# Optimization experiments

Hardware: AMD Instinct MI355X
Metric: run time of the kernel (lower is better)

The kernel has to match this reference:

```python
import jax, jax.numpy as jnp
import numpy as np

N_NODES = 50000  # nodes in the (sub)graph


def setup_inputs() -> dict:
    key = jax.random.key(0)
    ks = jax.random.split(key, 8)
    nodes = jax.random.randint(ks[0], (N_NODES,), 0, 100000)
    src = jax.random.randint(ks[1], (800000,), 0, N_NODES)
    dst = jax.random.randint(ks[2], (800000,), 0, N_NODES)
    emb = jax.random.normal(ks[3], (100000, 256), dtype=jnp.float32)
    W = jax.random.normal(ks[4], (256, 128), dtype=jnp.float32) * 0.05
    b = jax.random.normal(ks[5], (128,), dtype=jnp.float32) * 0.05
    mlp_w = jax.random.normal(ks[6], (128, 40), dtype=jnp.float32) * 0.05
    mlp_b = jax.random.normal(ks[7], (40,), dtype=jnp.float32) * 0.05
    return {"nodes": nodes, "src": src, "dst": dst, "emb": emb,
            "W": W, "b": b, "mlp_w": mlp_w, "mlp_b": mlp_b}


def reference(nodes, src, dst, emb, W, b, mlp_w, mlp_b):
    n = N_NODES
    ones = jnp.ones_like(src, dtype=jnp.float32)
    out_deg = jax.ops.segment_sum(ones, src, num_segments=n)  # src out-degree
    in_deg = jax.ops.segment_sum(ones, dst, num_segments=n)   # dst in-degree
    norm_src = jax.lax.rsqrt(jnp.maximum(out_deg, 1.0))       # D_out^{-1/2}
    norm_dst = jax.lax.rsqrt(jnp.maximum(in_deg, 1.0))        # D_in^{-1/2}

    feat = emb[nodes]                                          # [N, in_dim]
    # dgl GraphConv(norm='both'): in_dim > out_dim -> project first, then aggregate
    h = (feat * norm_src[:, None]) @ W                         # [N, out_dim]
    agg = jax.ops.segment_sum(h[src], dst, num_segments=n)     # SpMM: sum over in-edges
    feat_out = agg * norm_dst[:, None] + b                     # [N, out_dim]

    logits = feat_out @ mlp_w + mlp_b                          # [N, num_classes]
    return (feat_out, logits)
```

## Files before the change

kernel.cpp:

```cpp
#include <hip/hip_runtime.h>

#define IN_DIM 256
#define OUT_DIM 128
#define N_CLS 40

#define SLICE 16384
#define NE_CH 40

typedef __attribute__((ext_vector_type(8))) short short8;
typedef __attribute__((ext_vector_type(4))) float floatx4;

static __device__ __forceinline__ unsigned short f2bf(float f) {
    union { float f; unsigned u; } v; v.f = f;
    unsigned r = v.u + 0x7FFF + ((v.u >> 16) & 1);
    return (unsigned short)(r >> 16);
}

static __device__ __forceinline__ unsigned cvtpk(float lo, float hi) {
    unsigned r;
    asm("v_cvt_pk_bf16_f32 %0, %1, %2" : "=v"(r) : "v"(lo), "v"(hi));
    return r;
}

__global__ __launch_bounds__(256) void hist_wconv_kernel(
    const int* __restrict__ src, const int* __restrict__ dst,
    int* __restrict__ partial_out, int* __restrict__ partial_in,
    const float* __restrict__ W, unsigned short* __restrict__ Wt,
    int ne, int n, int chunk, int nbh)
{
    __shared__ __align__(16) int lh_out[SLICE];
    __shared__ __align__(16) int lh_in[SLICE];

    const int tid = threadIdx.x;

    if (blockIdx.x >= nbh) {
        int t = (blockIdx.x - nbh) * 256 + tid;
        if (t < IN_DIM * OUT_DIM) {
            int k = t >> 7, c = t & 127;
            Wt[c * IN_DIM + k] = f2bf(W[t]);
        }
        return;
    }

    const int s = blockIdx.x / NE_CH;
    const int e = blockIdx.x % NE_CH;
    const int lo = s * SLICE;
    const int hi = min(lo + SLICE, n);

    for (int i = tid; i < SLICE; i += 256) { lh_out[i] = 0; lh_in[i] = 0; }
    __syncthreads();

    const int start = e * chunk;
    const int end = min(start + chunk, ne);
    const int cnt4 = (end - start) >> 2;
    const int4* s4 = (const int4*)(src + start);
    const int4* d4 = (const int4*)(dst + start);
    for (int k = tid; k < cnt4; k += 256) {
        int4 sv = s4[k];
        int4 dv = d4[k];
        unsigned q;
        q = (unsigned)(sv.x - lo); if (q < SLICE) atomicAdd(&lh_out[q], 1);
        q = (unsigned)(sv.y - lo); if (q < SLICE) atomicAdd(&lh_out[q], 1);
        q = (unsigned)(sv.z - lo); if (q < SLICE) atomicAdd(&lh_out[q], 1);
        q = (unsigned)(sv.w - lo); if (q < SLICE) atomicAdd(&lh_out[q], 1);
        q = (unsigned)(dv.x - lo); if (q < SLICE) atomicAdd(&lh_in[q], 1);
        q = (unsigned)(dv.y - lo); if (q < SLICE) atomicAdd(&lh_in[q], 1);
        q = (unsigned)(dv.z - lo); if (q < SLICE) atomicAdd(&lh_in[q], 1);
        q = (unsigned)(dv.w - lo); if (q < SLICE) atomicAdd(&lh_in[q], 1);
    }
    for (int t = start + (cnt4 << 2) + tid; t < end; t += 256) {
        unsigned q;
        q = (unsigned)(src[t] - lo); if (q < SLICE) atomicAdd(&lh_out[q], 1);
        q = (unsigned)(dst[t] - lo); if (q < SLICE) atomicAdd(&lh_in[q], 1);
    }
    __syncthreads();

    const int cnt = hi - lo;
    const int c4 = cnt >> 2;
    int4* po = (int4*)(partial_out + (size_t)e * n + lo);
    int4* pi = (int4*)(partial_in + (size_t)e * n + lo);
    for (int i = tid; i < c4; i += 256) {
        po[i] = ((const int4*)lh_out)[i];
        pi[i] = ((const int4*)lh_in)[i];
    }
    for (int i = (c4 << 2) + tid; i < cnt; i += 256) {
        partial_out[(size_t)e * n + lo + i] = lh_out[i];
        partial_in[(size_t)e * n + lo + i] = lh_in[i];
    }
}

__global__ __launch_bounds__(256) void reduce_scan_kernel(
    int* __restrict__ partial_out, int* __restrict__ partial_in,
    int* __restrict__ cnt_out, int* __restrict__ row_start,
    int* __restrict__ bsum, int* __restrict__ boffs,
    int* __restrict__ done, int n)
{
    __shared__ int wsum[4];
    __shared__ int is_last;
    const int tid = threadIdx.x;
    const int lane = tid & 63, wid = tid >> 6;
    const int base = blockIdx.x * 1024 + tid * 4;

    int4 run = make_int4(0, 0, 0, 0);

    if (base + 4 <= n) {
        int4 sum = make_int4(0, 0, 0, 0);
#pragma unroll
        for (int e = 0; e < NE_CH; e++) {
            int4 v = *(const int4*)(partial_out + (size_t)e * n + base);
            sum.x += v.x; sum.y += v.y; sum.z += v.z; sum.w += v.w;
        }
        *(int4*)(cnt_out + base) = sum;

#pragma unroll
        for (int e = 0; e < NE_CH; e++) {
            int* p = partial_in + (size_t)e * n + base;
            int4 v = *(const int4*)p;
            *(int4*)p = run;
            run.x += v.x; run.y += v.y; run.z += v.z; run.w += v.w;
        }
    } else if (base <= n) {
        int rr[4] = {0, 0, 0, 0};
#pragma unroll
        for (int j = 0; j < 4; j++) {
            int pos = base + j;
            if (pos < n) {
                int sum = 0, r = 0;
                for (int e = 0; e < NE_CH; e++) {
                    sum += partial_out[(size_t)e * n + pos];
                    int v = partial_in[(size_t)e * n + pos];
                    partial_in[(size_t)e * n + pos] = r;
                    r += v;
                }
                cnt_out[pos] = sum;
                rr[j] = r;
            }
        }
        run.x = rr[0]; run.y = rr[1]; run.z = rr[2]; run.w = rr[3];
    }

    const int s = run.x + run.y + run.z + run.w;
    const int e1 = run.x, e2 = run.x + run.y, e3 = run.x + run.y + run.z;

    int incl = s;
#pragma unroll
    for (int off = 1; off < 64; off <<= 1) {
        int q = __shfl_up(incl, (unsigned)off, 64);
        if (lane >= off) incl += q;
    }
    if (lane == 63) wsum[wid] = incl;
    __syncthreads();
    int woff = 0;
    for (int w = 0; w < wid; ++w) woff += wsum[w];
    const int texcl = woff + incl - s;

    if (base + 4 <= n) {
        int4 o = make_int4(texcl, texcl + e1, texcl + e2, texcl + e3);
        *(int4*)(row_start + base) = o;
    } else if (base <= n) {
        const int eo[4] = {0, e1, e2, e3};
#pragma unroll
        for (int j = 0; j < 4; j++) {
            int pos = base + j;
            if (pos <= n) row_start[pos] = texcl + eo[j];
        }
    }
    if (tid == 0) bsum[blockIdx.x] = wsum[0] + wsum[1] + wsum[2] + wsum[3];

    __threadfence();
    if (tid == 0) {
        int prev = atomicAdd(done, 1);
        is_last = (prev == (int)gridDim.x - 1) ? 1 : 0;
    }
    __syncthreads();
    if (is_last && tid < 64) {
        __threadfence();
        const int nb = (int)gridDim.x;
        int carry = 0;
        for (int c = 0; c < nb; c += 64) {
            int i = c + lane;
            int v = (i < nb) ? bsum[i] : 0;
            int inc2 = v;
#pragma unroll
            for (int off = 1; off < 64; off <<= 1) {
                int q = __shfl_up(inc2, (unsigned)off, 64);
                if (lane >= off) inc2 += q;
            }
            if (i < nb) boffs[i] = carry + inc2 - v;
            carry += __shfl(inc2, 63, 64);
        }
        if (lane == 0) boffs[nb] = carry;
    }
}

__global__ __launch_bounds__(256) void scatter_lds_kernel(
    const int* __restrict__ src, const int* __restrict__ dst,
    const int* __restrict__ row_start, const int* __restrict__ boffs,
    const int* __restrict__ prefix_in,
    int* __restrict__ csr_src, int ne, int n, int chunk)
{
    __shared__ __align__(16) int cur[SLICE];

    const int tid = threadIdx.x;
    const int s = blockIdx.x / NE_CH;
    const int e = blockIdx.x % NE_CH;
    const int lo = s * SLICE;
    const int hi = min(lo + SLICE, n);
    const int cnt = hi - lo;

    const int c4 = cnt >> 2;
    for (int i = tid; i < c4; i += 256) {
        int idx4 = lo + i * 4;
        int4 rs = *(const int4*)(row_start + idx4);
        int4 pf = *(const int4*)(prefix_in + (size_t)e * n + idx4);
        const int bo = boffs[idx4 >> 10];
        rs.x += pf.x + bo; rs.y += pf.y + bo;
        rs.z += pf.z + bo; rs.w += pf.w + bo;
        ((int4*)cur)[i] = rs;
    }
    for (int i = (c4 << 2) + tid; i < cnt; i += 256) {
        int pos = lo + i;
        cur[i] = row_start[pos] + boffs[pos >> 10]
               + prefix_in[(size_t)e * n + pos];
    }
    __syncthreads();

    const int start = e * chunk;
    const int end = min(start + chunk, ne);
    const int cnt4e = (end - start) >> 2;
    const int4* s4 = (const int4*)(src + start);
    const int4* d4 = (const int4*)(dst + start);
    for (int k = tid; k < cnt4e; k += 256) {
        int4 sv = s4[k];
        int4 dv = d4[k];
        unsigned q;
        q = (unsigned)(dv.x - lo); if (q < SLICE) csr_src[atomicAdd(&cur[q], 1)] = sv.x;
        q = (unsigned)(dv.y - lo); if (q < SLICE) csr_src[atomicAdd(&cur[q], 1)] = sv.y;
        q = (unsigned)(dv.z - lo); if (q < SLICE) csr_src[atomicAdd(&cur[q], 1)] = sv.z;
        q = (unsigned)(dv.w - lo); if (q < SLICE) csr_src[atomicAdd(&cur[q], 1)] = sv.w;
    }
    for (int t = start + (cnt4e << 2) + tid; t < end; t += 256) {
        unsigned q = (unsigned)(dst[t] - lo);
        if (q < SLICE) csr_src[atomicAdd(&cur[q], 1)] = src[t];
    }
}

__global__ __launch_bounds__(256) void gemm1_mfma_kernel(
    const int* __restrict__ nodes, const float* __restrict__ emb,
    const unsigned short* __restrict__ Wt, const int* __restrict__ cnt_out,
    unsigned short* __restrict__ h, int n)
{
    __shared__ unsigned short A_lds[128 * 40];
    __shared__ unsigned short B_lds[128 * 40];
    __shared__ int   snode[128];
    __shared__ float sscale[128];

    const int tid = threadIdx.x;
    const int m0  = blockIdx.x * 128;

    if (tid < 128) {
        int gr = m0 + tid;
        snode[tid]  = (gr < n) ? nodes[gr] : 0;
        sscale[tid] = (gr < n) ? rsqrtf(fmaxf((float)cnt_out[gr], 1.0f)) : 0.0f;
    }
    __syncthreads();

    const int arow = tid >> 1, aq = tid & 1;
    const float* aptr = emb + (size_t)snode[arow] * IN_DIM + aq * 16;
    const unsigned short* bptr = Wt + arow * IN_DIM + aq * 16;

    float    ar[16];
    unsigned bw[8];

#define LOAD_REGS(KK) do {                                           \
        _Pragma("unroll")                                            \
        for (int q = 0; q < 4; q++) {                                \
            const floatx4 v = *(const floatx4*)(aptr + (KK) * 32 + q * 4); \
            ar[q*4+0]=v[0]; ar[q*4+1]=v[1]; ar[q*4+2]=v[2]; ar[q*4+3]=v[3]; \
        }                                                            \
        const uint4 w0 = *(const uint4*)(bptr + (KK) * 32);          \
        const uint4 w1 = *(const uint4*)(bptr + (KK) * 32 + 8);      \
        bw[0]=w0.x; bw[1]=w0.y; bw[2]=w0.z; bw[3]=w0.w;              \
        bw[4]=w1.x; bw[5]=w1.y; bw[6]=w1.z; bw[7]=w1.w;              \
    } while (0)

#define WRITE_LDS() do {                                             \
        uint4 uv0, uv1;                                              \
        uv0.x = cvtpk(ar[0],  ar[1]);  uv0.y = cvtpk(ar[2],  ar[3]); \
        uv0.z = cvtpk(ar[4],  ar[5]);  uv0.w = cvtpk(ar[6],  ar[7]); \
        uv1.x = cvtpk(ar[8],  ar[9]);  uv1.y = cvtpk(ar[10], ar[11]);\
        uv1.z = cvtpk(ar[12], ar[13]); uv1.w = cvtpk(ar[14], ar[15]);\
        *(uint4*)&A_lds[arow * 40 + aq * 16]     = uv0;              \
        *(uint4*)&A_lds[arow * 40 + aq * 16 + 8] = uv1;              \
        uint4 b0, b1;                                                \
        b0.x=bw[0]; b0.y=bw[1]; b0.z=bw[2]; b0.w=bw[3];              \
        b1.x=bw[4]; b1.y=bw[5]; b1.z=bw[6]; b1.w=bw[7];              \
        *(uint4*)&B_lds[arow * 40 + aq * 16]     = b0;               \
        *(uint4*)&B_lds[arow * 40 + aq * 16 + 8] = b1;               \
    } while (0)

    const int wave = tid >> 6, lane = tid & 63;
    const int wr = (wave & 1) * 64;
    const int wc = (wave >> 1) * 64;
    const int fr = lane & 15;
    const int koff = (lane >> 4) * 8;

    floatx4 acc[4][4];
#pragma unroll
    for (int i = 0; i < 4; i++)
#pragma unroll
        for (int j = 0; j < 4; j++) acc[i][j] = (floatx4){0.f, 0.f, 0.f, 0.f};

    LOAD_REGS(0);
    WRITE_LDS();

    for (int kk = 0; kk < 8; ++kk) {
        if (kk < 7) LOAD_REGS(kk + 1);
        __syncthreads();
        short8 af[4], bf[4];
#pragma unroll
        for (int t = 0; t < 4; t++) {
            af[t] = *(const short8*)&A_lds[(wr + t * 16 + fr) * 40 + koff];
            bf[t] = *(const short8*)&B_lds[(wc + t * 16 + fr) * 40 + koff];
        }
#pragma unroll
        for (int rt = 0; rt < 4; rt++)
#pragma unroll
            for (int ct = 0; ct < 4; ct++)
                acc[rt][ct] = __builtin_amdgcn_mfma_f32_16x16x32_bf16(
                    bf[ct], af[rt], acc[rt][ct], 0, 0, 0);
        __syncthreads();
        if (kk < 7) WRITE_LDS();
    }

#pragma unroll
    for (int rt = 0; rt < 4; rt++) {
        int lrow = wr + rt * 16 + fr;
        int grow = m0 + lrow;
        float sc = sscale[lrow];
        if (grow < n) {
#pragma unroll
            for (int ct = 0; ct < 4; ct++) {
                int col = wc + ct * 16 + (lane >> 4) * 4;
                uint2 o;
                o.x = cvtpk(acc[rt][ct][0] * sc, acc[rt][ct][1] * sc);
                o.y = cvtpk(acc[rt][ct][2] * sc, acc[rt][ct][3] * sc);
                *(uint2*)&h[(size_t)grow * OUT_DIM + col] = o;
            }
        }
    }
#undef LOAD_REGS
#undef WRITE_LDS
}

__global__ __launch_bounds__(256) void spmm_csr_kernel(
    const int* __restrict__ row_start, const int* __restrict__ boffs,
    const int* __restrict__ csr_src, const unsigned short* __restrict__ h,
    const float* __restrict__ bias, float* __restrict__ out_feat, int n)
{
    const int lane = threadIdx.x & 63;
    const int c2 = lane * 2;
    const int row = blockIdx.x * 4 + (threadIdx.x >> 6);
    if (row >= n) return;

    const int rs = row_start[row]     + boffs[row >> 10];
    const int re = row_start[row + 1] + boffs[(row + 1) >> 10];
    const int deg = re - rs;

    float aL[4] = {0.f, 0.f, 0.f, 0.f};
    float aH[4] = {0.f, 0.f, 0.f, 0.f};

    for (int base = 0; base < deg; base += 64) {
        const int cnt = min(deg - base, 64);
        int idx = (lane < cnt) ? csr_src[rs + base + lane] : 0;
        int t = 0;
        for (; t + 15 < cnt; t += 16) {
            int s[16];
#pragma unroll
            for (int u = 0; u < 16; u++) s[u] = __shfl(idx, t + u, 64);
            unsigned v[16];
#pragma unroll
            for (int u = 0; u < 16; u++)
                v[u] = *(const unsigned*)&h[(size_t)s[u] * OUT_DIM + c2];
#pragma unroll
            for (int u = 0; u < 16; u++) {
                union { unsigned uu; float f; } x, y;
                x.uu = v[u] << 16;
                y.uu = v[u] & 0xffff0000u;
                aL[u & 3] += x.f;
                aH[u & 3] += y.f;
            }
        }
        for (; t + 3 < cnt; t += 4) {
            int s[4];
#pragma unroll
            for (int u = 0; u < 4; u++) s[u] = __shfl(idx, t + u, 64);
            unsigned v[4];
#pragma unroll
            for (int u = 0; u < 4; u++)
                v[u] = *(const unsigned*)&h[(size_t)s[u] * OUT_DIM + c2];
#pragma unroll
            for (int u = 0; u < 4; u++) {
                union { unsigned uu; float f; } x, y;
                x.uu = v[u] << 16;
                y.uu = v[u] & 0xffff0000u;
                aL[u] += x.f;
                aH[u] += y.f;
            }
        }
        for (; t < cnt; ++t) {
            int s0 = __shfl(idx, t, 64);
            unsigned v0 = *(const unsigned*)&h[(size_t)s0 * OUT_DIM + c2];
            union { unsigned uu; float f; } x, y;
            x.uu = v0 << 16;
            y.uu = v0 & 0xffff0000u;
            aL[0] += x.f;
            aH[0] += y.f;
        }
    }

    const float nd = rsqrtf(fmaxf((float)deg, 1.0f));
    const float f0 = ((aL[0] + aL[1]) + (aL[2] + aL[3])) * nd + bias[c2];
    const float f1 = ((aH[0] + aH[1]) + (aH[2] + aH[3])) * nd + bias[c2 + 1];
    union { float f[2]; unsigned long long u; } o;
    o.f[0] = f0; o.f[1] = f1;
    __builtin_nontemporal_store(o.u,
        (unsigned long long*)&out_feat[(size_t)row * OUT_DIM + c2]);
}

__global__ __launch_bounds__(256) void mlp_mfma_kernel(
    const float* __restrict__ F, const float* __restrict__ mlp_w,
    const float* __restrict__ mlp_b, float* __restrict__ out_logits, int n)
{
    __shared__ unsigned short A_lds[48 * 136];
    __shared__ float s_mlpb[48];

    const int tid = threadIdx.x;
    for (int i = tid; i < 48 * 128; i += 256) {
        int cls = i >> 7, k = i & 127;
        A_lds[cls * 136 + k] =
            (cls < N_CLS) ? f2bf(mlp_w[(size_t)k * N_CLS + cls]) : (unsigned short)0;
    }
    if (tid < 48) s_mlpb[tid] = (tid < N_CLS) ? mlp_b[tid] : 0.f;
    __syncthreads();

    const int wave = tid >> 6, lane = tid & 63;
    const int r = lane & 15, koff = (lane >> 4) * 8;
    const int row = blockIdx.x * 64 + wave * 16 + r;
    const int rowc = (row < n) ? row : (n - 1);
    const float* fp = F + (size_t)rowc * OUT_DIM + koff;

    floatx4 acc[3];
#pragma unroll
    for (int ct = 0; ct < 3; ct++) acc[ct] = (floatx4){0.f, 0.f, 0.f, 0.f};

#pragma unroll
    for (int kk = 0; kk < 4; kk++) {
        floatx4 v0 = *(const floatx4*)(fp + kk * 32);
        floatx4 v1 = *(const floatx4*)(fp + kk * 32 + 4);
        union { unsigned u32[4]; short8 v; } bfr;
        bfr.u32[0] = cvtpk(v0[0], v0[1]);
        bfr.u32[1] = cvtpk(v0[2], v0[3]);
        bfr.u32[2] = cvtpk(v1[0], v1[1]);
        bfr.u32[3] = cvtpk(v1[2], v1[3]);
#pragma unroll
        for (int ct = 0; ct < 3; ct++) {
            short8 af = *(const short8*)&A_lds[(ct * 16 + r) * 136 + kk * 32 + koff];
            acc[ct] = __builtin_amdgcn_mfma_f32_16x16x32_bf16(af, bfr.v, acc[ct], 0, 0, 0);
        }
    }

    if (row < n) {
#pragma unroll
        for (int ct = 0; ct < 3; ct++)
#pragma unroll
            for (int i = 0; i < 4; i++) {
                int cls = ct * 16 + (lane >> 4) * 4 + i;
                if (cls < N_CLS)
                    __builtin_nontemporal_store(acc[ct][i] + s_mlpb[cls],
                        &out_logits[(size_t)row * N_CLS + cls]);
            }
    }
}

extern "C" void kernel_launch(void* const* d_in, const int* in_sizes, int n_in,
                              void* d_out, int out_size, void* d_ws, size_t ws_size,
                              hipStream_t stream) {
    const int*   nodes = (const int*)d_in[0];
    const int*   src   = (const int*)d_in[1];
    const int*   dst   = (const int*)d_in[2];
    const float* emb   = (const float*)d_in[3];
    const float* W     = (const float*)d_in[4];
    const float* b     = (const float*)d_in[5];
    const float* mlp_w = (const float*)d_in[6];
    const float* mlp_b = (const float*)d_in[7];

    const int n  = in_sizes[0];
    const int ne = in_sizes[1];

    int* cnt_out     = (int*)d_ws;
    int* bsum        = cnt_out + n;
    int* boffs       = bsum + 512;
    int* done        = boffs + 512;
    int* row_start   = done + 8;
    int* csr_src     = row_start + n + 8;
    int* partial_out = csr_src + ne;
    int* partial_in  = partial_out + (size_t)NE_CH * n;
    size_t off = ((size_t)(2 * n + 1048) + (size_t)ne + 2 * (size_t)NE_CH * n) * sizeof(int);
    off = (off + 15) & ~(size_t)15;
    unsigned short* Wt = (unsigned short*)((char*)d_ws + off);
    off += (size_t)IN_DIM * OUT_DIM * sizeof(unsigned short);
    off = (off + 15) & ~(size_t)15;
    unsigned short* h = (unsigned short*)((char*)d_ws + off);

    float* out_feat   = (float*)d_out;
    float* out_logits = out_feat + (size_t)n * OUT_DIM;

    const int ns = (n + SLICE - 1) / SLICE;
    const int chunk = (((ne + NE_CH - 1) / NE_CH) + 3) & ~3;
    const int nbh = ns * NE_CH;
    const int nbw = (IN_DIM * OUT_DIM + 255) / 256;
    const int nb = (n + 1023) / 1024;

    hipMemsetAsync(done, 0, sizeof(int), stream);

    hist_wconv_kernel<<<nbh + nbw, 256, 0, stream>>>(
        src, dst, partial_out, partial_in, W, Wt, ne, n, chunk, nbh);
    reduce_scan_kernel<<<nb, 256, 0, stream>>>(
        partial_out, partial_in, cnt_out, row_start, bsum, boffs, done, n);
    gemm1_mfma_kernel<<<(n + 127) / 128, 256, 0, stream>>>(
        nodes, emb, Wt, cnt_out, h, n);
    scatter_lds_kernel<<<nbh, 256, 0, stream>>>(
        src, dst, row_start, boffs, partial_in, csr_src, ne, n, chunk);
    spmm_csr_kernel<<<(n + 3) / 4, 256, 0, stream>>>(
        row_start, boffs, csr_src, h, b, out_feat, n);
    mlp_mfma_kernel<<<(n + 63) / 64, 256, 0, stream>>>(
        out_feat, mlp_w, mlp_b, out_logits, n);
}
```

Measured before the change: 135.4 us.

## Merge CSR scatter and gather-GEMM into one launch; reset counter in hist kernel

Combines the CSR scatter kernel and the embedding-gather GEMM into a single launch by splitting the grid: the first nbh blocks do the LDS-cursor scatter and the rest do the MFMA projection, sharing one 64KB shared buffer. The hipMemsetAsync that zeroed the scan's done counter is dropped, and the first weight-conversion block of the histogram kernel resets it instead. This removes one launch and one memset and lets the scatter and GEMM blocks run at the same time. The cost is that GEMM blocks now reserve 64KB of LDS, which can lower their occupancy.

After: 126.4 us. 6.7% less time.

```diff
diff --git a/kernel.cpp b/kernel.cpp
--- a/kernel.cpp
+++ b/kernel.cpp
@@ -26,7 +26,7 @@
     const int* __restrict__ src, const int* __restrict__ dst,
     int* __restrict__ partial_out, int* __restrict__ partial_in,
     const float* __restrict__ W, unsigned short* __restrict__ Wt,
-    int ne, int n, int chunk, int nbh)
+    int* __restrict__ done, int ne, int n, int chunk, int nbh)
 {
     __shared__ __align__(16) int lh_out[SLICE];
     __shared__ __align__(16) int lh_in[SLICE];
@@ -34,6 +34,7 @@
     const int tid = threadIdx.x;
 
     if (blockIdx.x >= nbh) {
+        if (blockIdx.x == (unsigned)nbh && tid == 0) *done = 0;
         int t = (blockIdx.x - nbh) * 256 + tid;
         if (t < IN_DIM * OUT_DIM) {
             int k = t >> 7, c = t & 127;
@@ -193,70 +194,71 @@
     }
 }
 
-__global__ __launch_bounds__(256) void scatter_lds_kernel(
+__global__ __launch_bounds__(256) void scatter_gemm_kernel(
     const int* __restrict__ src, const int* __restrict__ dst,
     const int* __restrict__ row_start, const int* __restrict__ boffs,
-    const int* __restrict__ prefix_in,
-    int* __restrict__ csr_src, int ne, int n, int chunk)
-{
-    __shared__ __align__(16) int cur[SLICE];
-
-    const int tid = threadIdx.x;
-    const int s = blockIdx.x / NE_CH;
-    const int e = blockIdx.x % NE_CH;
-    const int lo = s * SLICE;
-    const int hi = min(lo + SLICE, n);
-    const int cnt = hi - lo;
-
-    const int c4 = cnt >> 2;
-    for (int i = tid; i < c4; i += 256) {
-        int idx4 = lo + i * 4;
-        int4 rs = *(const int4*)(row_start + idx4);
-        int4 pf = *(const int4*)(prefix_in + (size_t)e * n + idx4);
-        const int bo = boffs[idx4 >> 10];
-        rs.x += pf.x + bo; rs.y += pf.y + bo;
-        rs.z += pf.z + bo; rs.w += pf.w + bo;
-        ((int4*)cur)[i] = rs;
-    }
-    for (int i = (c4 << 2) + tid; i < cnt; i += 256) {
-        int pos = lo + i;
-        cur[i] = row_start[pos] + boffs[pos >> 10]
-               + prefix_in[(size_t)e * n + pos];
-    }
-    __syncthreads();
-
-    const int start = e * chunk;
-    const int end = min(start + chunk, ne);
-    const int cnt4e = (end - start) >> 2;
-    const int4* s4 = (const int4*)(src + start);
-    const int4* d4 = (const int4*)(dst + start);
-    for (int k = tid; k < cnt4e; k += 256) {
-        int4 sv = s4[k];
-        int4 dv = d4[k];
-        unsigned q;
-        q = (unsigned)(dv.x - lo); if (q < SLICE) csr_src[atomicAdd(&cur[q], 1)] = sv.x;
-        q = (unsigned)(dv.y - lo); if (q < SLICE) csr_src[atomicAdd(&cur[q], 1)] = sv.y;
-        q = (unsigned)(dv.z - lo); if (q < SLICE) csr_src[atomicAdd(&cur[q], 1)] = sv.z;
-        q = (unsigned)(dv.w - lo); if (q < SLICE) csr_src[atomicAdd(&cur[q], 1)] = sv.w;
-    }
-    for (int t = start + (cnt4e << 2) + tid; t < end; t += 256) {
-        unsigned q = (unsigned)(dst[t] - lo);
-        if (q < SLICE) csr_src[atomicAdd(&cur[q], 1)] = src[t];
-    }
-}
-
-__global__ __launch_bounds__(256) void gemm1_mfma_kernel(
+    const int* __restrict__ prefix_in, int* __restrict__ csr_src,
     const int* __restrict__ nodes, const float* __restrict__ emb,
     const unsigned short* __restrict__ Wt, const int* __restrict__ cnt_out,
-    unsigned short* __restrict__ h, int n)
+    unsigned short* __restrict__ h,
+    int ne, int n, int chunk, int nbh)
 {
-    __shared__ unsigned short A_lds[128 * 40];
-    __shared__ unsigned short B_lds[128 * 40];
-    __shared__ int   snode[128];
-    __shared__ float sscale[128];
+    __shared__ __align__(16) char smem[SLICE * 4];
 
     const int tid = threadIdx.x;
-    const int m0  = blockIdx.x * 128;
+
+    if (blockIdx.x < (unsigned)nbh) {
+        int* cur = (int*)smem;
+        const int s = blockIdx.x / NE_CH;
+        const int e = blockIdx.x % NE_CH;
+        const int lo = s * SLICE;
+        const int hi = min(lo + SLICE, n);
+        const int cnt = hi - lo;
+
+        const int c4 = cnt >> 2;
+        for (int i = tid; i < c4; i += 256) {
+            int idx4 = lo + i * 4;
+            int4 rs = *(const int4*)(row_start + idx4);
+            int4 pf = *(const int4*)(prefix_in + (size_t)e * n + idx4);
+            const int bo = boffs[idx4 >> 10];
+            rs.x += pf.x + bo; rs.y += pf.y + bo;
+            rs.z += pf.z + bo; rs.w += pf.w + bo;
+            ((int4*)cur)[i] = rs;
+        }
+        for (int i = (c4 << 2) + tid; i < cnt; i += 256) {
+            int pos = lo + i;
+            cur[i] = row_start[pos] + boffs[pos >> 10]
+                   + prefix_in[(size_t)e * n + pos];
+        }
+        __syncthreads();
+
+        const int start = e * chunk;
+        const int end = min(start + chunk, ne);
+        const int cnt4e = (end - start) >> 2;
+        const int4* s4 = (const int4*)(src + start);
+        const int4* d4 = (const int4*)(dst + start);
+        for (int k = tid; k < cnt4e; k += 256) {
+            int4 sv = s4[k];
+            int4 dv = d4[k];
+            unsigned q;
+            q = (unsigned)(dv.x - lo); if (q < SLICE) csr_src[atomicAdd(&cur[q], 1)] = sv.x;
+            q = (unsigned)(dv.y - lo); if (q < SLICE) csr_src[atomicAdd(&cur[q], 1)] = sv.y;
+            q = (unsigned)(dv.z - lo); if (q < SLICE) csr_src[atomicAdd(&cur[q], 1)] = sv.z;
+            q = (unsigned)(dv.w - lo); if (q < SLICE) csr_src[atomicAdd(&cur[q], 1)] = sv.w;
+        }
+        for (int t = start + (cnt4e << 2) + tid; t < end; t += 256) {
+            unsigned q = (unsigned)(dst[t] - lo);
+            if (q < SLICE) csr_src[atomicAdd(&cur[q], 1)] = src[t];
+        }
+        return;
+    }
+
+    unsigned short* A_lds = (unsigned short*)smem;
+    unsigned short* B_lds = (unsigned short*)(smem + 10240);
+    int*   snode  = (int*)(smem + 20480);
+    float* sscale = (float*)(smem + 20992);
+
+    const int m0 = (blockIdx.x - nbh) * 128;
 
     if (tid < 128) {
         int gr = m0 + tid;
@@ -521,17 +523,15 @@
     const int nbh = ns * NE_CH;
     const int nbw = (IN_DIM * OUT_DIM + 255) / 256;
     const int nb = (n + 1023) / 1024;
-
-    hipMemsetAsync(done, 0, sizeof(int), stream);
+    const int ngb = (n + 127) / 128;
 
     hist_wconv_kernel<<<nbh + nbw, 256, 0, stream>>>(
-        src, dst, partial_out, partial_in, W, Wt, ne, n, chunk, nbh);
+        src, dst, partial_out, partial_in, W, Wt, done, ne, n, chunk, nbh);
     reduce_scan_kernel<<<nb, 256, 0, stream>>>(
         partial_out, partial_in, cnt_out, row_start, bsum, boffs, done, n);
-    gemm1_mfma_kernel<<<(n + 127) / 128, 256, 0, stream>>>(
-        nodes, emb, Wt, cnt_out, h, n);
-    scatter_lds_kernel<<<nbh, 256, 0, stream>>>(
-        src, dst, row_start, boffs, partial_in, csr_src, ne, n, chunk);
+    scatter_gemm_kernel<<<nbh + ngb, 256, 0, stream>>>(
+        src, dst, row_start, boffs, partial_in, csr_src,
+        nodes, emb, Wt, cnt_out, h, ne, n, chunk, nbh);
     spmm_csr_kernel<<<(n + 3) / 4, 256, 0, stream>>>(
         row_start, boffs, csr_src, h, b, out_feat, n);
     mlp_mfma_kernel<<<(n + 63) / 64, 256, 0, stream>>>(
```
